# Kernel optimization log

Measured on AMD Instinct MI355X. Metric: run time of the kernel, lower is better.

## Reference

```python
import jax, jax.numpy as jnp
import numpy as np

NEG_SLOPE = 0.2  # PyG GATConv default LeakyReLU slope
EPS = 1e-16


def gat_layer(x, W, a_src, a_dst, bias, src, dst, heads, out_dim, concat):
    N = x.shape[0]
    h = (x @ W).reshape(N, heads, out_dim)          # [N,H,C]
    alpha_src = (h * a_src).sum(-1)                  # [N,H]
    alpha_dst = (h * a_dst).sum(-1)                  # [N,H]
    e = jax.nn.leaky_relu(alpha_src[src] + alpha_dst[dst], NEG_SLOPE)  # [E,H]
    # segment softmax over incoming edges of each destination node
    m = jax.ops.segment_max(e, dst, num_segments=N)  # [N,H]
    p = jnp.exp(e - m[dst])
    denom = jax.ops.segment_sum(p, dst, num_segments=N)
    alpha = p / (denom[dst] + EPS)                   # [E,H]
    # scatter-aggregate messages to destinations
    out = jax.ops.segment_sum(alpha[:, :, None] * h[src], dst, num_segments=N)  # [N,H,C]
    out = out.reshape(N, heads * out_dim) if concat else out.mean(axis=1)
    return out + bias


def setup_inputs() -> dict:
    N, E, F_IN, NC = 100000, 1600000, 512, 10
    key = jax.random.key(0)
    ks = jax.random.split(key, 9)
    return {
        "x": jax.random.normal(ks[0], (N, F_IN), jnp.float32),
        "W1": jax.random.normal(ks[1], (F_IN, 64), jnp.float32) * (1.0 / np.sqrt(F_IN)),
        "att_src1": jax.random.normal(ks[2], (1, 8, 8), jnp.float32) * 0.1,
        "att_dst1": jax.random.normal(ks[3], (1, 8, 8), jnp.float32) * 0.1,
        "b1": jnp.zeros((64,), jnp.float32),
        "W2": jax.random.normal(ks[4], (64, NC), jnp.float32) * (1.0 / 8.0),
        "att_src2": jax.random.normal(ks[5], (1, 1, NC), jnp.float32) * 0.1,
        "att_dst2": jax.random.normal(ks[6], (1, 1, NC), jnp.float32) * 0.1,
        "b2": jnp.zeros((NC,), jnp.float32),
        "edge_index": jax.random.randint(ks[7], (2, E), 0, N, jnp.int64),
    }


def reference(x, W1, att_src1, att_dst1, b1, W2, att_src2, att_dst2, b2, edge_index):
    N = x.shape[0]
    # add self-loops (PyG GATConv add_self_loops=True default)
    loop = jnp.arange(N, dtype=edge_index.dtype)
    src = jnp.concatenate([edge_index[0], loop])
    dst = jnp.concatenate([edge_index[1], loop])
    h = gat_layer(x, W1, att_src1, att_dst1, b1, src, dst, heads=8, out_dim=8, concat=True)
    h = jax.nn.elu(h)
    nc = W2.shape[1]
    out = gat_layer(h, W2, att_src2, att_dst2, b2, src, dst, heads=1, out_dim=nc, concat=False)
    return jax.nn.log_softmax(out, axis=1)
```

## Files before the change

kernel.cpp:

```cpp
#include <hip/hip_runtime.h>
#include <math.h>

#define NEG 0.2f

__global__ __launch_bounds__(256) void gemm1_k(const float* __restrict__ x,
                                               const float* __restrict__ W1,
                                               float* __restrict__ h1, int Nn)
{
    const int TK = 32;
    __shared__ float xs[TK][68];
    __shared__ float ws[TK][68];
    int row0 = blockIdx.x * 64;
    int t = threadIdx.x;
    int tr = t >> 4, tc = t & 15;
    float acc[4][4] = {};
    for (int kb = 0; kb < 512; kb += TK) {
#pragma unroll
        for (int i = 0; i < 2; ++i) {
            int idx = t + 256 * i;
            int r = idx >> 3;
            int k4 = idx & 7;
            float4 v = make_float4(0.f, 0.f, 0.f, 0.f);
            int gr = row0 + r;
            if (gr < Nn) v = *(const float4*)(x + (size_t)gr * 512 + kb + k4 * 4);
            xs[k4 * 4 + 0][r] = v.x;
            xs[k4 * 4 + 1][r] = v.y;
            xs[k4 * 4 + 2][r] = v.z;
            xs[k4 * 4 + 3][r] = v.w;
        }
#pragma unroll
        for (int i = 0; i < 2; ++i) {
            int idx = t + 256 * i;
            int k = idx >> 4;
            int c4 = idx & 15;
            *(float4*)&ws[k][c4 * 4] =
                *(const float4*)(W1 + (size_t)(kb + k) * 64 + c4 * 4);
        }
        __syncthreads();
#pragma unroll
        for (int kk = 0; kk < TK; ++kk) {
            float4 a = *(const float4*)&xs[kk][tr * 4];
            float4 b = *(const float4*)&ws[kk][tc * 4];
            acc[0][0] += a.x * b.x; acc[0][1] += a.x * b.y; acc[0][2] += a.x * b.z; acc[0][3] += a.x * b.w;
            acc[1][0] += a.y * b.x; acc[1][1] += a.y * b.y; acc[1][2] += a.y * b.z; acc[1][3] += a.y * b.w;
            acc[2][0] += a.z * b.x; acc[2][1] += a.z * b.y; acc[2][2] += a.z * b.z; acc[2][3] += a.z * b.w;
            acc[3][0] += a.w * b.x; acc[3][1] += a.w * b.y; acc[3][2] += a.w * b.z; acc[3][3] += a.w * b.w;
        }
        __syncthreads();
    }
#pragma unroll
    for (int i = 0; i < 4; ++i) {
        int gr = row0 + tr * 4 + i;
        if (gr < Nn) {
            float4 v = make_float4(acc[i][0], acc[i][1], acc[i][2], acc[i][3]);
            *(float4*)(h1 + (size_t)gr * 64 + tc * 4) = v;
        }
    }
}

__global__ void attn1_k(const float* __restrict__ h1, const float* __restrict__ asrc,
                        const float* __restrict__ adst, float* __restrict__ as1,
                        float* __restrict__ ad1, int Nn)
{
    int tid = blockIdx.x * 256 + threadIdx.x;
    if (tid >= Nn * 8) return;
    int n = tid >> 3, h = tid & 7;
    const float* hp = h1 + (size_t)n * 64 + h * 8;
    float s = 0.f, d = 0.f;
#pragma unroll
    for (int c = 0; c < 8; ++c) {
        float v = hp[c];
        s += v * asrc[h * 8 + c];
        d += v * adst[h * 8 + c];
    }
    as1[tid] = s;
    ad1[tid] = d;
}

__global__ void hist_rank_k(const int* __restrict__ ei, int E, int Nn,
                            int* __restrict__ deg, int* __restrict__ rank)
{
    int e = blockIdx.x * 256 + threadIdx.x;
    int Ep = E + Nn;
    if (e >= Ep) return;
    int d = (e < E) ? ei[E + e] : e - E;
    rank[e] = atomicAdd(&deg[d], 1);
}

__global__ void scan_a_k(const int* __restrict__ deg, int Nn, int* __restrict__ bsum)
{
    __shared__ int tmp[256];
    int t = threadIdx.x;
    int base = blockIdx.x * 1024 + t * 4;
    int s = 0;
#pragma unroll
    for (int j = 0; j < 4; ++j) { int i = base + j; if (i < Nn) s += deg[i]; }
    tmp[t] = s;
    __syncthreads();
    for (int off = 1; off < 256; off <<= 1) {
        int a = (t >= off) ? tmp[t - off] : 0;
        __syncthreads();
        tmp[t] += a;
        __syncthreads();
    }
    if (t == 255) bsum[blockIdx.x] = tmp[255];
}

__global__ void scan_b_k(int* __restrict__ bsum, int nb)
{
    __shared__ int tmp[256];
    int t = threadIdx.x;
    int v = (t < nb) ? bsum[t] : 0;
    tmp[t] = v;
    __syncthreads();
    for (int off = 1; off < 256; off <<= 1) {
        int a = (t >= off) ? tmp[t - off] : 0;
        __syncthreads();
        tmp[t] += a;
        __syncthreads();
    }
    if (t < nb) bsum[t] = tmp[t] - v;
}

__global__ void scan_c_k(const int* __restrict__ deg, int Nn, const int* __restrict__ boff,
                         int* __restrict__ rowptr)
{
    __shared__ int tmp[256];
    int t = threadIdx.x;
    int base = blockIdx.x * 1024 + t * 4;
    int v[4];
    int s = 0;
#pragma unroll
    for (int j = 0; j < 4; ++j) {
        int i = base + j;
        v[j] = (i < Nn) ? deg[i] : 0;
        s += v[j];
    }
    tmp[t] = s;
    __syncthreads();
    for (int off = 1; off < 256; off <<= 1) {
        int a = (t >= off) ? tmp[t - off] : 0;
        __syncthreads();
        tmp[t] += a;
        __syncthreads();
    }
    int excl = boff[blockIdx.x] + tmp[t] - s;
#pragma unroll
    for (int j = 0; j < 4; ++j) {
        int i = base + j;
        if (i < Nn) {
            rowptr[i] = excl;
            excl += v[j];
            if (i == Nn - 1) rowptr[Nn] = excl;
        }
    }
}

__global__ void scat2_k(const int* __restrict__ ei, int E, int Nn,
                        const int* __restrict__ rowptr, const int* __restrict__ rank,
                        int* __restrict__ csr)
{
    int e = blockIdx.x * 256 + threadIdx.x;
    int Ep = E + Nn;
    if (e >= Ep) return;
    int s, d;
    if (e < E) { s = ei[e]; d = ei[E + e]; } else { s = d = e - E; }
    csr[rowptr[d] + rank[e]] = s;
}

__global__ __launch_bounds__(256) void agg1_k(const int* __restrict__ csr,
                                              const int* __restrict__ rowptr,
                                              const float* __restrict__ as1,
                                              const float* __restrict__ ad1,
                                              const float* __restrict__ h1,
                                              float* __restrict__ out1, int Nn)
{
    int wid = (blockIdx.x * 256 + threadIdx.x) >> 6;
    if (wid >= Nn) return;
    int lane = threadIdx.x & 63;
    int sub = lane >> 4;
    int c4 = lane & 15;
    int h = c4 >> 1;
    float adv = ad1[wid * 8 + h];
    int start = rowptr[wid];
    int len = rowptr[wid + 1] - start;
    float accp = 0.f;
    float4 accv = make_float4(0.f, 0.f, 0.f, 0.f);
    int i = sub;
    for (; i + 12 < len; i += 16) {
        int s0 = csr[start + i];
        int s1 = csr[start + i + 4];
        int s2 = csr[start + i + 8];
        int s3 = csr[start + i + 12];
        float e0 = as1[s0 * 8 + h] + adv;
        float e1 = as1[s1 * 8 + h] + adv;
        float e2 = as1[s2 * 8 + h] + adv;
        float e3 = as1[s3 * 8 + h] + adv;
        float4 hv0 = *(const float4*)(h1 + (size_t)s0 * 64 + c4 * 4);
        float4 hv1 = *(const float4*)(h1 + (size_t)s1 * 64 + c4 * 4);
        float4 hv2 = *(const float4*)(h1 + (size_t)s2 * 64 + c4 * 4);
        float4 hv3 = *(const float4*)(h1 + (size_t)s3 * 64 + c4 * 4);
        e0 = e0 > 0.f ? e0 : NEG * e0;
        e1 = e1 > 0.f ? e1 : NEG * e1;
        e2 = e2 > 0.f ? e2 : NEG * e2;
        e3 = e3 > 0.f ? e3 : NEG * e3;
        float p0 = __expf(e0), p1 = __expf(e1), p2 = __expf(e2), p3 = __expf(e3);
        accp += (p0 + p1) + (p2 + p3);
        accv.x += p0 * hv0.x + p1 * hv1.x + p2 * hv2.x + p3 * hv3.x;
        accv.y += p0 * hv0.y + p1 * hv1.y + p2 * hv2.y + p3 * hv3.y;
        accv.z += p0 * hv0.z + p1 * hv1.z + p2 * hv2.z + p3 * hv3.z;
        accv.w += p0 * hv0.w + p1 * hv1.w + p2 * hv2.w + p3 * hv3.w;
    }
    for (; i < len; i += 4) {
        int s0 = csr[start + i];
        float e0 = as1[s0 * 8 + h] + adv;
        float4 hv0 = *(const float4*)(h1 + (size_t)s0 * 64 + c4 * 4);
        e0 = e0 > 0.f ? e0 : NEG * e0;
        float p0 = __expf(e0);
        accp += p0;
        accv.x += p0 * hv0.x;
        accv.y += p0 * hv0.y;
        accv.z += p0 * hv0.z;
        accv.w += p0 * hv0.w;
    }
    accp   += __shfl_xor(accp, 16);
    accv.x += __shfl_xor(accv.x, 16);
    accv.y += __shfl_xor(accv.y, 16);
    accv.z += __shfl_xor(accv.z, 16);
    accv.w += __shfl_xor(accv.w, 16);
    accp   += __shfl_xor(accp, 32);
    accv.x += __shfl_xor(accv.x, 32);
    accv.y += __shfl_xor(accv.y, 32);
    accv.z += __shfl_xor(accv.z, 32);
    accv.w += __shfl_xor(accv.w, 32);
    if (sub == 0) {
        float inv = 1.f / (accp + 1e-16f);
        float4 o = make_float4(accv.x * inv, accv.y * inv, accv.z * inv, accv.w * inv);
        *(float4*)(out1 + (size_t)wid * 64 + c4 * 4) = o;
    }
}

__global__ void node2_k(const float* __restrict__ out1, const float* __restrict__ b1,
                        const float* __restrict__ W2, const float* __restrict__ as2w,
                        const float* __restrict__ ad2w, float* __restrict__ h2,
                        float* __restrict__ as2, float* __restrict__ ad2, int Nn)
{
    int n = blockIdx.x * 256 + threadIdx.x;
    if (n >= Nn) return;
    float g[64];
#pragma unroll
    for (int c = 0; c < 16; ++c) {
        float4 v = *(const float4*)(out1 + (size_t)n * 64 + c * 4);
        float4 b = *(const float4*)(b1 + c * 4);
        float t0 = v.x + b.x, t1 = v.y + b.y, t2 = v.z + b.z, t3 = v.w + b.w;
        g[c * 4 + 0] = t0 > 0.f ? t0 : expm1f(t0);
        g[c * 4 + 1] = t1 > 0.f ? t1 : expm1f(t1);
        g[c * 4 + 2] = t2 > 0.f ? t2 : expm1f(t2);
        g[c * 4 + 3] = t3 > 0.f ? t3 : expm1f(t3);
    }
    float acc[10] = {};
#pragma unroll
    for (int k = 0; k < 64; ++k) {
#pragma unroll
        for (int j = 0; j < 10; ++j) acc[j] += g[k] * W2[k * 10 + j];
    }
    float s = 0.f, d = 0.f;
#pragma unroll
    for (int j = 0; j < 10; ++j) {
        h2[(size_t)n * 16 + j] = acc[j];
        s += acc[j] * as2w[j];
        d += acc[j] * ad2w[j];
    }
    as2[n] = s;
    ad2[n] = d;
}

__global__ __launch_bounds__(256) void agg2_k(const int* __restrict__ csr,
                                              const int* __restrict__ rowptr,
                                              const float* __restrict__ as2,
                                              const float* __restrict__ ad2,
                                              const float* __restrict__ h2,
                                              float* __restrict__ out, int Nn)
{
    int wid = (blockIdx.x * 256 + threadIdx.x) >> 6;
    if (wid >= Nn) return;
    int lane = threadIdx.x & 63;
    int sub = lane >> 4;
    int c = lane & 15;
    float adv = ad2[wid];
    int start = rowptr[wid];
    int len = rowptr[wid + 1] - start;
    float accp = 0.f, accv = 0.f;
    int i = sub;
    for (; i + 12 < len; i += 16) {
        int s0 = csr[start + i];
        int s1 = csr[start + i + 4];
        int s2 = csr[start + i + 8];
        int s3 = csr[start + i + 12];
        float e0 = as2[s0] + adv;
        float e1 = as2[s1] + adv;
        float e2 = as2[s2] + adv;
        float e3 = as2[s3] + adv;
        float v0 = (c < 10) ? h2[(size_t)s0 * 16 + c] : 0.f;
        float v1 = (c < 10) ? h2[(size_t)s1 * 16 + c] : 0.f;
        float v2 = (c < 10) ? h2[(size_t)s2 * 16 + c] : 0.f;
        float v3 = (c < 10) ? h2[(size_t)s3 * 16 + c] : 0.f;
        e0 = e0 > 0.f ? e0 : NEG * e0;
        e1 = e1 > 0.f ? e1 : NEG * e1;
        e2 = e2 > 0.f ? e2 : NEG * e2;
        e3 = e3 > 0.f ? e3 : NEG * e3;
        float p0 = __expf(e0), p1 = __expf(e1), p2 = __expf(e2), p3 = __expf(e3);
        accp += (p0 + p1) + (p2 + p3);
        accv += p0 * v0 + p1 * v1 + p2 * v2 + p3 * v3;
    }
    for (; i < len; i += 4) {
        int s0 = csr[start + i];
        float e0 = as2[s0] + adv;
        float v0 = (c < 10) ? h2[(size_t)s0 * 16 + c] : 0.f;
        e0 = e0 > 0.f ? e0 : NEG * e0;
        float p0 = __expf(e0);
        accp += p0;
        accv += p0 * v0;
    }
    accp += __shfl_xor(accp, 16);
    accv += __shfl_xor(accv, 16);
    accp += __shfl_xor(accp, 32);
    accv += __shfl_xor(accv, 32);
    if (sub == 0 && c < 10)
        out[(size_t)wid * 10 + c] = accv / (accp + 1e-16f);
}

__global__ void lsm_k(float* __restrict__ out, const float* __restrict__ b2, int Nn)
{
    int n = blockIdx.x * 256 + threadIdx.x;
    if (n >= Nn) return;
    float z[10];
    float m = -1e30f;
#pragma unroll
    for (int j = 0; j < 10; ++j) {
        z[j] = out[(size_t)n * 10 + j] + b2[j];
        m = fmaxf(m, z[j]);
    }
    float ssum = 0.f;
#pragma unroll
    for (int j = 0; j < 10; ++j) ssum += expf(z[j] - m);
    float lse = m + logf(ssum);
#pragma unroll
    for (int j = 0; j < 10; ++j) out[(size_t)n * 10 + j] = z[j] - lse;
}

extern "C" void kernel_launch(void* const* d_in, const int* in_sizes, int n_in,
                              void* d_out, int out_size, void* d_ws, size_t ws_size,
                              hipStream_t stream)
{
    const float* x     = (const float*)d_in[0];
    const float* W1    = (const float*)d_in[1];
    const float* asrc1 = (const float*)d_in[2];
    const float* adst1 = (const float*)d_in[3];
    const float* b1    = (const float*)d_in[4];
    const float* W2    = (const float*)d_in[5];
    const float* asrc2 = (const float*)d_in[6];
    const float* adst2 = (const float*)d_in[7];
    const float* b2    = (const float*)d_in[8];
    const int*   ei    = (const int*)d_in[9];
    float* out = (float*)d_out;

    int F  = in_sizes[1] / 64;
    int Nn = in_sizes[0] / F;
    int E  = in_sizes[9] / 2;
    int Ep = E + Nn;
    int nb = (Nn + 1023) / 1024;

    float* f = (float*)d_ws;
    float* h1   = f;  f += (size_t)Nn * 64;
    float* as1  = f;  f += (size_t)Nn * 8;
    float* ad1  = f;  f += (size_t)Nn * 8;
    float* h2   = f;  f += (size_t)Nn * 16;
    float* as2  = f;  f += Nn;
    float* ad2  = f;  f += Nn;
    float* out1 = f;  f += (size_t)Nn * 64;
    int* ip = (int*)f;
    int* deg    = ip;  ip += Nn;
    int* rowptr = ip;  ip += Nn + 1;
    int* bsum   = ip;  ip += 256;
    int* rank   = ip;  ip += Ep;
    int* csr    = ip;  ip += Ep;

    hipMemsetAsync(deg, 0, (size_t)Nn * sizeof(int), stream);
    hist_rank_k<<<(Ep + 255) / 256, 256, 0, stream>>>(ei, E, Nn, deg, rank);
    scan_a_k<<<nb, 256, 0, stream>>>(deg, Nn, bsum);
    scan_b_k<<<1, 256, 0, stream>>>(bsum, nb);
    scan_c_k<<<nb, 256, 0, stream>>>(deg, Nn, bsum, rowptr);
    scat2_k<<<(Ep + 255) / 256, 256, 0, stream>>>(ei, E, Nn, rowptr, rank, csr);

    gemm1_k<<<(Nn + 63) / 64, 256, 0, stream>>>(x, W1, h1, Nn);
    attn1_k<<<(Nn * 8 + 255) / 256, 256, 0, stream>>>(h1, asrc1, adst1, as1, ad1, Nn);
    agg1_k<<<(Nn * 64 + 255) / 256, 256, 0, stream>>>(csr, rowptr, as1, ad1, h1, out1, Nn);

    node2_k<<<(Nn + 255) / 256, 256, 0, stream>>>(out1, b1, W2, asrc2, adst2, h2, as2, ad2, Nn);
    agg2_k<<<(Nn * 64 + 255) / 256, 256, 0, stream>>>(csr, rowptr, as2, ad2, h2, out, Nn);
    lsm_k<<<(Nn + 255) / 256, 256, 0, stream>>>(out, b2, Nn);
}
```

Before: 602.4 us.

## Use bf16 MFMA for first-layer GEMM with double-buffered shared tiles

Rewrites the x@W1 GEMM to convert inputs to bf16 and use the 16x16x32 bf16 MFMA instruction, with W1 fragments held in registers and x tiles double-buffered in shared memory. The goal is to replace scalar FP32 FMA work with matrix-core throughput and overlap global loads with compute. It reduces input precision to bf16, which may affect accuracy. It also raises register pressure because 16 bf16x8 B fragments are kept live.

```diff
diff --git a/kernel.cpp b/kernel.cpp
--- a/kernel.cpp
+++ b/kernel.cpp
@@ -2,58 +2,80 @@
 #include <math.h>
 
 #define NEG 0.2f
+
+typedef __bf16 bf16x4 __attribute__((ext_vector_type(4)));
+typedef __bf16 bf16x8 __attribute__((ext_vector_type(8)));
+typedef float  f32x4  __attribute__((ext_vector_type(4)));
 
 __global__ __launch_bounds__(256) void gemm1_k(const float* __restrict__ x,
                                                const float* __restrict__ W1,
                                                float* __restrict__ h1, int Nn)
 {
-    const int TK = 32;
-    __shared__ float xs[TK][68];
-    __shared__ float ws[TK][68];
+    __shared__ __bf16 xs[2][64][40];
+    int t = threadIdx.x;
+    int wave = t >> 6, lane = t & 63;
     int row0 = blockIdx.x * 64;
-    int t = threadIdx.x;
-    int tr = t >> 4, tc = t & 15;
-    float acc[4][4] = {};
-    for (int kb = 0; kb < 512; kb += TK) {
-#pragma unroll
-        for (int i = 0; i < 2; ++i) {
-            int idx = t + 256 * i;
-            int r = idx >> 3;
-            int k4 = idx & 7;
+    int col0 = wave * 16;
+    int lm = lane & 15;
+    int lk = lane >> 4;
+
+    bf16x8 bfrag[16];
+#pragma unroll
+    for (int ch = 0; ch < 16; ++ch) {
+        int kb = ch * 32 + lk * 8;
+#pragma unroll
+        for (int j = 0; j < 8; ++j)
+            bfrag[ch][j] = (__bf16)W1[(size_t)(kb + j) * 64 + col0 + lm];
+    }
+
+    f32x4 acc[4] = {};
+
+    {
+        int r = t >> 3, c4 = t & 7;
+#pragma unroll
+        for (int p = 0; p < 2; ++p) {
+            int rr = p * 32 + r;
+            int gr = row0 + rr;
             float4 v = make_float4(0.f, 0.f, 0.f, 0.f);
-            int gr = row0 + r;
-            if (gr < Nn) v = *(const float4*)(x + (size_t)gr * 512 + kb + k4 * 4);
-            xs[k4 * 4 + 0][r] = v.x;
-            xs[k4 * 4 + 1][r] = v.y;
-            xs[k4 * 4 + 2][r] = v.z;
-            xs[k4 * 4 + 3][r] = v.w;
+            if (gr < Nn) v = *(const float4*)(x + (size_t)gr * 512 + c4 * 4);
+            bf16x4 b;
+            b[0] = (__bf16)v.x; b[1] = (__bf16)v.y; b[2] = (__bf16)v.z; b[3] = (__bf16)v.w;
+            *(bf16x4*)&xs[0][rr][c4 * 4] = b;
         }
-#pragma unroll
-        for (int i = 0; i < 2; ++i) {
-            int idx = t + 256 * i;
-            int k = idx >> 4;
-            int c4 = idx & 15;
-            *(float4*)&ws[k][c4 * 4] =
-                *(const float4*)(W1 + (size_t)(kb + k) * 64 + c4 * 4);
+    }
+    __syncthreads();
+
+#pragma unroll
+    for (int ch = 0; ch < 16; ++ch) {
+        int buf = ch & 1;
+        if (ch < 15) {
+            int kb = (ch + 1) * 32;
+            int r = t >> 3, c4 = t & 7;
+#pragma unroll
+            for (int p = 0; p < 2; ++p) {
+                int rr = p * 32 + r;
+                int gr = row0 + rr;
+                float4 v = make_float4(0.f, 0.f, 0.f, 0.f);
+                if (gr < Nn) v = *(const float4*)(x + (size_t)gr * 512 + kb + c4 * 4);
+                bf16x4 b;
+                b[0] = (__bf16)v.x; b[1] = (__bf16)v.y; b[2] = (__bf16)v.z; b[3] = (__bf16)v.w;
+                *(bf16x4*)&xs[1 - buf][rr][c4 * 4] = b;
+            }
         }
-        __syncthreads();
-#pragma unroll
-        for (int kk = 0; kk < TK; ++kk) {
-            float4 a = *(const float4*)&xs[kk][tr * 4];
-            float4 b = *(const float4*)&ws[kk][tc * 4];
-            acc[0][0] += a.x * b.x; acc[0][1] += a.x * b.y; acc[0][2] += a.x * b.z; acc[0][3] += a.x * b.w;
-            acc[1][0] += a.y * b.x; acc[1][1] += a.y * b.y; acc[1][2] += a.y * b.z; acc[1][3] += a.y * b.w;
-            acc[2][0] += a.z * b.x; acc[2][1] += a.z * b.y; acc[2][2] += a.z * b.z; acc[2][3] += a.z * b.w;
-            acc[3][0] += a.w * b.x; acc[3][1] += a.w * b.y; acc[3][2] += a.w * b.z; acc[3][3] += a.w * b.w;
+#pragma unroll
+        for (int rt = 0; rt < 4; ++rt) {
+            bf16x8 a = *(bf16x8*)&xs[buf][rt * 16 + lm][lk * 8];
+            acc[rt] = __builtin_amdgcn_mfma_f32_16x16x32_bf16(a, bfrag[ch], acc[rt], 0, 0, 0);
         }
         __syncthreads();
     }
-#pragma unroll
-    for (int i = 0; i < 4; ++i) {
-        int gr = row0 + tr * 4 + i;
-        if (gr < Nn) {
-            float4 v = make_float4(acc[i][0], acc[i][1], acc[i][2], acc[i][3]);
-            *(float4*)(h1 + (size_t)gr * 64 + tc * 4) = v;
+
+#pragma unroll
+    for (int rt = 0; rt < 4; ++rt) {
+#pragma unroll
+        for (int j = 0; j < 4; ++j) {
+            int gr = row0 + rt * 16 + lk * 4 + j;
+            if (gr < Nn) h1[(size_t)gr * 64 + col0 + lm] = acc[rt][j];
         }
     }
 }
```

After: 607.3 us. Within noise of the previous version (+0.8%).
